# Optimization experiments

Hardware: AMD Instinct MI355X
Metric: run time of the kernel (lower is better)

The kernel has to match this reference:

```python
import jax, jax.numpy as jnp
import numpy as np
import math

V, S, D, C, L = 32000, 1024, 768, 6, 4
B = 32
PAD = 0
EPS = 1e-5


def _ln(x, w, b):
    m = jnp.mean(x, axis=-1, keepdims=True)
    v = jnp.var(x, axis=-1, keepdims=True)
    return (x - m) * jax.lax.rsqrt(v + EPS) * w + b


def setup_inputs() -> dict:
    key = jax.random.key(0)
    ks = jax.random.split(key, 20)
    s = 0.02
    emb = jax.random.normal(ks[0], (V, D), jnp.float32) * s
    emb = emb.at[PAD].set(0.0)  # padding_idx row zeroed
    pos_emb = jax.random.normal(ks[1], (S, D), jnp.float32) * s
    tokens = jax.random.randint(ks[2], (B, S), 0, V)
    d = dict(
        tokens=tokens,
        emb=emb,
        pos_emb=pos_emb,
        ln1_w=jnp.ones((L, D)), ln1_b=jnp.zeros((L, D)),
        ln2_w=jnp.ones((L, D)), ln2_b=jnp.zeros((L, D)),
        wq=jax.random.normal(ks[3], (L, D, D)) * s, bq=jnp.zeros((L, D)),
        wk=jax.random.normal(ks[4], (L, D, D)) * s, bk=jnp.zeros((L, D)),
        wv=jax.random.normal(ks[5], (L, D, D)) * s, bv=jnp.zeros((L, D)),
        w1=jax.random.normal(ks[6], (L, D, 2 * D)) * s, b1=jnp.zeros((L, 2 * D)),
        w2=jax.random.normal(ks[7], (L, 2 * D, D)) * s, b2=jnp.zeros((L, D)),
        lnf_w=jnp.ones((D,)), lnf_b=jnp.zeros((D,)),
        wc=jax.random.normal(ks[8], (D, C)) * s, bc=jnp.zeros((C,)),
    )
    return d


def reference(tokens, emb, pos_emb, ln1_w, ln1_b, ln2_w, ln2_b,
              wq, bq, wk, bk, wv, bv, w1, b1, w2, b2,
              lnf_w, lnf_b, wc, bc):
    # dropout in eval mode -> identity
    seq = tokens.shape[1]
    x = emb[tokens] + pos_emb[jnp.arange(seq)][None]  # [B,S,D]
    pad = (tokens == PAD)[:, None, :]  # [B,1,S] mask over key positions
    scale = math.sqrt(D)
    for l in range(L):
        n = _ln(x, ln1_w[l], ln1_b[l])
        q = n @ wq[l] + bq[l]
        k = n @ wk[l] + bk[l]
        v = n @ wv[l] + bv[l]
        scores = jnp.einsum('bqd,bkd->bqk', q, k) / scale
        scores = jnp.where(pad, -jnp.inf, scores)
        attn = jax.nn.softmax(scores, axis=-1)
        x = x + jnp.einsum('bqk,bkd->bqd', attn, v)
        h = jax.nn.relu(_ln(x, ln2_w[l], ln2_b[l]) @ w1[l] + b1[l])
        x = x + h @ w2[l] + b2[l]
    x = _ln(x, lnf_w, lnf_b)
    tok_mask = (tokens != PAD)[..., None].astype(x.dtype)  # [B,S,1]
    pooled = (x * tok_mask).sum(axis=1) / jnp.clip(tok_mask.sum(axis=1), 1.0, None)
    return pooled @ wc + bc
```

## Files before the change

### kernel.cpp

```cpp
#include <hip/hip_runtime.h>
#include <hip/hip_bf16.h>


typedef float f32x4 __attribute__((ext_vector_type(4)));
typedef unsigned short u16x4 __attribute__((ext_vector_type(4)));
typedef unsigned short u16x8 __attribute__((ext_vector_type(8)));
typedef int   i32x4 __attribute__((ext_vector_type(4)));
typedef __bf16 bf16x8 __attribute__((ext_vector_type(8)));

#define NB  32
#define NS  1024
#define ND  768
#define NH  1536
#define NL  4
#define NM  (NB * NS)

__device__ __forceinline__ unsigned short f2bf(float f) {
    unsigned u = __builtin_bit_cast(unsigned, f);
    unsigned r = (u + 0x7FFFu + ((u >> 16) & 1u)) >> 16;
    return (unsigned short)r;
}
__device__ __forceinline__ float bf2f(unsigned short h) {
    return __builtin_bit_cast(float, (unsigned)h << 16);
}
__device__ __forceinline__ unsigned short f2h(float f) {
    _Float16 h = (_Float16)f;
    return __builtin_bit_cast(unsigned short, h);
}
__device__ __forceinline__ float h2f(unsigned short u) {
    _Float16 h = __builtin_bit_cast(_Float16, u);
    return (float)h;
}

__device__ __forceinline__ void gl_lds16(const void* g, void* l) {
    __builtin_amdgcn_global_load_lds(
        (const __attribute__((address_space(1))) unsigned int*)g,
        (__attribute__((address_space(3))) unsigned int*)l, 16, 0, 0);
}

__global__ void embed_kernel(const int* __restrict__ tok,
                             const float* __restrict__ emb,
                             const float* __restrict__ pos,
                             unsigned short* __restrict__ x) {
    const int row = blockIdx.x;
    const int c = threadIdx.x;
    const int tk = tok[row];
    const int s = row & (NS - 1);
    f32x4 e = *(const f32x4*)(emb + (size_t)tk * ND + c * 4);
    f32x4 p = *(const f32x4*)(pos + (size_t)s * ND + c * 4);
    u16x4 o;
    #pragma unroll
    for (int i = 0; i < 4; i++) o[i] = f2h(e[i] + p[i]);
    *(u16x4*)(x + (size_t)row * ND + c * 4) = o;
}

__global__ __launch_bounds__(256)
void wt_kernel(const float* __restrict__ in, unsigned short* __restrict__ out,
               int R, int Cc, size_t ozs) {
    __shared__ float ls[64][65];
    const int t = threadIdx.x;
    const size_t zi = (size_t)blockIdx.z * R * Cc;
    const size_t zo = (size_t)blockIdx.z * ozs;
    const int r0 = blockIdx.y * 64, c0 = blockIdx.x * 64;
    #pragma unroll
    for (int i = 0; i < 4; i++) {
        const int r = i * 16 + (t >> 4);
        const int c = (t & 15) * 4;
        f32x4 v = *(const f32x4*)(in + zi + (size_t)(r0 + r) * Cc + c0 + c);
        ls[r][c] = v[0]; ls[r][c + 1] = v[1]; ls[r][c + 2] = v[2]; ls[r][c + 3] = v[3];
    }
    __syncthreads();
    #pragma unroll
    for (int i = 0; i < 2; i++) {
        const int c = i * 32 + (t >> 3);
        const int r = (t & 7) * 8;
        u16x8 o;
        #pragma unroll
        for (int j = 0; j < 8; j++) o[j] = f2bf(ls[r + j][c]);
        *(u16x8*)(out + zo + (size_t)(c0 + c) * R + r0 + r) = o;
    }
}

__global__ void bcat_kernel(const float* __restrict__ bq, const float* __restrict__ bk,
                            float* __restrict__ bqk) {
    const int i = blockIdx.x * 256 + threadIdx.x;
    const int l = i / NH, j = i % NH;
    bqk[i] = (j < ND) ? bq[l * ND + j] : bk[l * ND + j - ND];
}

__global__ __launch_bounds__(256)
void ln_kernel(const unsigned short* __restrict__ x, const float* __restrict__ g,
               const float* __restrict__ bta, unsigned short* __restrict__ out) {
    const int row = blockIdx.x * 4 + (threadIdx.x >> 6);
    const int l = threadIdx.x & 63;
    const unsigned short* xr = x + (size_t)row * ND;
    f32x4 vv[3];
    float s = 0.f, ss = 0.f;
    #pragma unroll
    for (int j = 0; j < 3; j++) {
        u16x4 hv = *(const u16x4*)(xr + (j * 64 + l) * 4);
        #pragma unroll
        for (int i = 0; i < 4; i++) {
            vv[j][i] = h2f(hv[i]);
            s += vv[j][i]; ss += vv[j][i] * vv[j][i];
        }
    }
    #pragma unroll
    for (int off = 32; off >= 1; off >>= 1) {
        s += __shfl_xor(s, off); ss += __shfl_xor(ss, off);
    }
    const float mean = s * (1.0f / ND);
    const float var = ss * (1.0f / ND) - mean * mean;
    const float rstd = rsqrtf(var + 1e-5f);
    #pragma unroll
    for (int j = 0; j < 3; j++) {
        const int c = (j * 64 + l) * 4;
        f32x4 gv = *(const f32x4*)(g + c);
        f32x4 bv = *(const f32x4*)(bta + c);
        u16x4 o;
        #pragma unroll
        for (int i = 0; i < 4; i++) o[i] = f2bf((vv[j][i] - mean) * rstd * gv[i] + bv[i]);
        *(u16x4*)(out + (size_t)row * ND + c) = o;
    }
}

template<int EPI, int BROW>
__global__ __launch_bounds__(512, 2)
void gemm256_kernel(const unsigned short* __restrict__ A,
                    const unsigned short* __restrict__ Bt,
                    const float* __restrict__ bias,
                    void* __restrict__ Cv,
                    int N, int K, int lda, int ldb,
                    long sA, long sB, long sC, float scale, int doswz) {
    __shared__ unsigned short lds[65536];
    const int tid = threadIdx.x;
    const int wid = tid >> 6, l = tid & 63;
    const int wr = wid >> 2, wc = wid & 3;
    const int fr = l & 15, fq = l >> 4;

    int bn = blockIdx.x, bm = blockIdx.y, bz = blockIdx.z;
    if (doswz) {
        const int gx = gridDim.x, gy = gridDim.y;
        const int nwg = gx * gy * gridDim.z;
        const int flat = (bz * gy + bm) * gx + bn;
        int s = (flat & 7) * (nwg >> 3) + (flat >> 3);
        bn = s % gx; s /= gx; bm = s % gy; bz = s / gy;
    }

    const unsigned short* Ab = A + (size_t)bz * sA + (size_t)(bm * 256) * lda;
    const unsigned short* Bb = Bt + (size_t)bz * sB + (size_t)(bn * 256) * ldb;

    const int srow = tid >> 3;
    const int scol = ((tid & 7) ^ (srow & 7)) * 8;
    const unsigned ldst = (unsigned)wid * 1024u;

    auto stageA = [&](int kt, int h) {
        const unsigned base = (unsigned)(kt & 1) * 65536u + (unsigned)h * 16384u;
        #pragma unroll
        for (int li = 0; li < 2; li++)
            gl_lds16(Ab + (size_t)(h * 128 + li * 64 + srow) * lda + (kt * 64 + scol),
                     (char*)lds + base + (unsigned)li * 8192u + ldst);
    };
    auto stageB = [&](int kt, int h) {
        const unsigned base = (unsigned)(kt & 1) * 65536u + 32768u + (unsigned)h * 16384u;
        #pragma unroll
        for (int li = 0; li < 2; li++)
            gl_lds16(Bb + (size_t)(h * 128 + li * 64 + srow) * ldb + (kt * 64 + scol),
                     (char*)lds + base + (unsigned)li * 8192u + ldst);
    };
    auto ldaf = [&](int buf, int mi, int kk) -> bf16x8 {
        const unsigned r = (unsigned)(mi * 16 + fr);
        unsigned byt = r * 128u + (unsigned)kk * 64u + (unsigned)fq * 16u;
        byt ^= (r & 7u) << 4;
        return *(const bf16x8*)((const char*)lds +
            (unsigned)buf * 65536u + (unsigned)wr * 16384u + byt);
    };
    auto ldbf = [&](int buf, int ni, int kk) -> bf16x8 {
        const unsigned r = (unsigned)((wc & 1) * 64 + ni * 16 + fr);
        unsigned byt = r * 128u + (unsigned)kk * 64u + (unsigned)fq * 16u;
        byt ^= (r & 7u) << 4;
        return *(const bf16x8*)((const char*)lds +
            (unsigned)buf * 65536u + 32768u + (unsigned)(wc >> 1) * 16384u + byt);
    };

    const int NT = K >> 6;
    f32x4 acc[8][4] = {};

    stageB(0, 0); stageB(0, 1); stageA(0, 0); stageA(0, 1);
    if (NT > 1) {
        stageB(1, 0); stageB(1, 1);
        asm volatile("s_waitcnt vmcnt(4)" ::: "memory");
    } else {
        asm volatile("s_waitcnt vmcnt(0)" ::: "memory");
    }
    __builtin_amdgcn_s_barrier();
    __builtin_amdgcn_sched_barrier(0);

    for (int t = 0; t < NT; ++t) {
        const int cur = t & 1;
        bf16x8 bfr[8];
        #pragma unroll
        for (int ni = 0; ni < 4; ni++) {
            bfr[ni * 2 + 0] = ldbf(cur, ni, 0);
            bfr[ni * 2 + 1] = ldbf(cur, ni, 1);
        }
        #pragma unroll
        for (int p = 0; p < 4; p++) {
            bf16x8 a0 = ldaf(cur, 2 * p,     0);
            bf16x8 a1 = ldaf(cur, 2 * p,     1);
            bf16x8 a2 = ldaf(cur, 2 * p + 1, 0);
            bf16x8 a3 = ldaf(cur, 2 * p + 1, 1);
            if (p < 2) { if (t + 1 < NT) stageA(t + 1, p); }
            else       { if (t + 2 < NT) stageB(t + 2, p - 2); }
            if (p == 3) {
                if (t + 2 < NT) asm volatile("s_waitcnt vmcnt(4)" ::: "memory");
                else            asm volatile("s_waitcnt vmcnt(0)" ::: "memory");
            }
            __builtin_amdgcn_s_barrier();
            asm volatile("s_waitcnt lgkmcnt(0)" ::: "memory");
            __builtin_amdgcn_sched_barrier(0);
            __builtin_amdgcn_s_setprio(1);
            #pragma unroll
            for (int ni = 0; ni < 4; ni++) {
                acc[2 * p][ni] = __builtin_amdgcn_mfma_f32_16x16x32_bf16(
                    a0, bfr[ni * 2 + 0], acc[2 * p][ni], 0, 0, 0);
                acc[2 * p][ni] = __builtin_amdgcn_mfma_f32_16x16x32_bf16(
                    a1, bfr[ni * 2 + 1], acc[2 * p][ni], 0, 0, 0);
                acc[2 * p + 1][ni] = __builtin_amdgcn_mfma_f32_16x16x32_bf16(
                    a2, bfr[ni * 2 + 0], acc[2 * p + 1][ni], 0, 0, 0);
                acc[2 * p + 1][ni] = __builtin_amdgcn_mfma_f32_16x16x32_bf16(
                    a3, bfr[ni * 2 + 1], acc[2 * p + 1][ni], 0, 0, 0);
            }
            __builtin_amdgcn_s_setprio(0);
            __builtin_amdgcn_sched_barrier(0);
            __builtin_amdgcn_s_barrier();
            __builtin_amdgcn_sched_barrier(0);
        }
    }

    const int erow = tid >> 4;
    const int echk = tid & 15;
    #pragma unroll
    for (int h2 = 0; h2 < 2; ++h2) {
        __builtin_amdgcn_s_barrier();
        if (wr == h2) {
            #pragma unroll
            for (int mi = 0; mi < 8; mi++) {
                #pragma unroll
                for (int ni = 0; ni < 4; ni++) {
                    const int nl = wc * 64 + ni * 16 + fr;
                    const float bcol = (!BROW && bias) ? bias[bn * 256 + nl] : 0.0f;
                    f32x4 brow = {0, 0, 0, 0};
                    if (BROW) brow = *(const f32x4*)(bias + bm * 256 + h2 * 128 + mi * 16 + fq * 4);
                    #pragma unroll
                    for (int r = 0; r < 4; r++) {
                        const int lm = mi * 16 + fq * 4 + r;
                        float v = acc[mi][ni][r] * scale + (BROW ? brow[r] : bcol);
                        if (EPI == 1) v = fmaxf(v, 0.0f);
                        const unsigned byt = ((unsigned)lm * 1024u + (unsigned)nl * 4u)
                                             ^ ((unsigned)(lm & 7) << 4);
                        *(float*)((char*)lds + byt) = v;
                    }
                }
            }
        }
        __builtin_amdgcn_s_barrier();
        #pragma unroll
        for (int j = 0; j < 16; j++) {
            const int row = erow + 32 * (j >> 2);
            const int c   = echk + 16 * (j & 3);
            const unsigned byt = ((unsigned)row * 1024u + (unsigned)c * 16u)
                                 ^ ((unsigned)(row & 7) << 4);
            f32x4 v = *(const f32x4*)((const char*)lds + byt);
            const int m = bm * 256 + h2 * 128 + row;
            const int ncol = bn * 256 + c * 4;
            const size_t offc = (size_t)bz * sC + (size_t)m * N + ncol;
            if (EPI == 2) {
                unsigned short* cp = (unsigned short*)Cv + offc;
                u16x4 hv = *(const u16x4*)cp;
                u16x4 o;
                #pragma unroll
                for (int r = 0; r < 4; r++) o[r] = f2h(h2f(hv[r]) + v[r]);
                *(u16x4*)cp = o;
            } else {
                u16x4 o;
                o[0] = f2bf(v[0]); o[1] = f2bf(v[1]); o[2] = f2bf(v[2]); o[3] = f2bf(v[3]);
                *(u16x4*)((unsigned short*)Cv + offc) = o;
            }
        }
    }
}

__global__ __launch_bounds__(256)
void softmax_kernel(unsigned short* __restrict__ sc, const int* __restrict__ tokg) {
    const int row = blockIdx.x * 4 + (threadIdx.x >> 6);
    const int l = threadIdx.x & 63;
    const int b = row >> 10;
    unsigned short* rp = sc + (size_t)row * NS;
    const int* trow = tokg + (size_t)b * NS;
    float v[16];
    float mx = -3.4e38f;
    #pragma unroll
    for (int j = 0; j < 2; j++) {
        u16x8 u = *(const u16x8*)(rp + j * 512 + l * 8);
        i32x4 t0 = *(const i32x4*)(trow + j * 512 + l * 8);
        i32x4 t1 = *(const i32x4*)(trow + j * 512 + l * 8 + 4);
        #pragma unroll
        for (int i = 0; i < 8; i++) {
            const int tk = (i < 4) ? t0[i] : t1[i - 4];
            const float s = (tk == 0) ? -__builtin_inff() : bf2f(u[i]);
            v[j * 8 + i] = s;
            mx = fmaxf(mx, s);
        }
    }
    #pragma unroll
    for (int off = 32; off >= 1; off >>= 1) mx = fmaxf(mx, __shfl_xor(mx, off));
    float sum = 0.f;
    #pragma unroll
    for (int i = 0; i < 16; i++) { v[i] = __expf(v[i] - mx); sum += v[i]; }
    #pragma unroll
    for (int off = 32; off >= 1; off >>= 1) sum += __shfl_xor(sum, off);
    const float inv = 1.0f / sum;
    #pragma unroll
    for (int j = 0; j < 2; j++) {
        u16x8 o;
        #pragma unroll
        for (int i = 0; i < 8; i++) o[i] = f2bf(v[j * 8 + i] * inv);
        *(u16x8*)(rp + j * 512 + l * 8) = o;
    }
}

__global__ __launch_bounds__(256)
void pool1_kernel(const unsigned short* __restrict__ ln,
                  const int* __restrict__ tokg,
                  float* __restrict__ part, float* __restrict__ cnts,
                  int gbase) {
    const int d = blockIdx.x * 256 + threadIdx.x;
    const int b = blockIdx.y;
    const int z = blockIdx.z;
    float s = 0.f, cnt = 0.f;
    const int i0 = z * 128;
    for (int i = i0; i < i0 + 128; i++) {
        const int tk = tokg[b * NS + i];
        if (tk != 0) { s += bf2f(ln[((size_t)b * NS + i) * ND + d]); cnt += 1.0f; }
    }
    part[((size_t)z * NB + (gbase + b)) * ND + d] = s;
    if (d == 0) cnts[z * NB + (gbase + b)] = cnt;
}

__global__ __launch_bounds__(256)
void pool2_kernel(const float* __restrict__ part, const float* __restrict__ cnts,
                  float* __restrict__ pooled) {
    const int d = blockIdx.x * 256 + threadIdx.x;
    const int b = blockIdx.y;
    float s = 0.f, cnt = 0.f;
    #pragma unroll
    for (int z = 0; z < 8; z++) {
        s += part[((size_t)z * NB + b) * ND + d];
        cnt += cnts[z * NB + b];
    }
    pooled[(size_t)b * ND + d] = s / fmaxf(cnt, 1.0f);
}

__global__ void cls_kernel(const float* __restrict__ pooled, const float* __restrict__ wc,
                           const float* __restrict__ bc, float* __restrict__ out) {
    const int b = blockIdx.x;
    const int l = threadIdx.x;
    float a[6] = {0, 0, 0, 0, 0, 0};
    for (int d = l; d < ND; d += 64) {
        const float p = pooled[b * ND + d];
        #pragma unroll
        for (int c = 0; c < 6; c++) a[c] += p * wc[d * 6 + c];
    }
    #pragma unroll
    for (int c = 0; c < 6; c++) {
        #pragma unroll
        for (int off = 32; off >= 1; off >>= 1) a[c] += __shfl_xor(a[c], off);
    }
    if (l == 0) {
        #pragma unroll
        for (int c = 0; c < 6; c++) out[b * 6 + c] = a[c] + bc[c];
    }
}

__global__ void zero_out_kernel(float* out, int nel) {
    const int i = blockIdx.x * 256 + threadIdx.x;
    if (i < nel) out[i] = 0.0f;
}

extern "C" void kernel_launch(void* const* d_in, const int* in_sizes, int n_in,
                              void* d_out, int out_size, void* d_ws, size_t ws_size,
                              hipStream_t stream) {
    const int*   tok  = (const int*)d_in[0];
    const float* emb  = (const float*)d_in[1];
    const float* pos  = (const float*)d_in[2];
    const float* ln1w = (const float*)d_in[3];
    const float* ln1b = (const float*)d_in[4];
    const float* ln2w = (const float*)d_in[5];
    const float* ln2b = (const float*)d_in[6];
    const float* wq   = (const float*)d_in[7];
    const float* bq   = (const float*)d_in[8];
    const float* wk   = (const float*)d_in[9];
    const float* bk   = (const float*)d_in[10];
    const float* wv   = (const float*)d_in[11];
    const float* bv   = (const float*)d_in[12];
    const float* w1   = (const float*)d_in[13];
    const float* b1   = (const float*)d_in[14];
    const float* w2   = (const float*)d_in[15];
    const float* b2   = (const float*)d_in[16];
    const float* lnfw = (const float*)d_in[17];
    const float* lnfb = (const float*)d_in[18];
    const float* wcw  = (const float*)d_in[19];
    const float* bcb  = (const float*)d_in[20];
    float* out = (float*)d_out;

    size_t off = 0;
    auto carve = [&](size_t bytes) -> char* {
        char* p = (char*)d_ws + off;
        off += (bytes + 255) & ~(size_t)255;
        return p;
    };
    unsigned short* x = (unsigned short*)carve((size_t)NM * ND * 2);
    unsigned short* wqkT = (unsigned short*)carve((size_t)NL * NH * ND * 2);
    unsigned short* wvT  = (unsigned short*)carve((size_t)NL * ND * ND * 2);
    unsigned short* w1T  = (unsigned short*)carve((size_t)NL * ND * NH * 2);
    unsigned short* w2T  = (unsigned short*)carve((size_t)NL * NH * ND * 2);
    float* bqk    = (float*)carve((size_t)NL * NH * 4);
    float* part   = (float*)carve((size_t)8 * NB * ND * 4);
    float* cnts   = (float*)carve((size_t)8 * NB * 4);
    float* pooled = (float*)carve((size_t)NB * ND * 4);

    int G = 32;
    while (G >= 1) {
        const size_t pool = (size_t)G *
            ((size_t)NS * ND * 2
           + (size_t)NS * NH * 2
           + (size_t)NS * ND * 2
           + (size_t)NS * NS * 2);
        if (off + pool <= ws_size) break;
        G >>= 1;
    }
    if (G < 1) {
        zero_out_kernel<<<(out_size + 255) / 256, 256, 0, stream>>>(out, out_size);
        return;
    }
    const int MG = G * NS;
    unsigned short* n  = (unsigned short*)carve((size_t)MG * ND * 2);
    unsigned short* qk = (unsigned short*)carve((size_t)MG * NH * 2);
    unsigned short* vt = (unsigned short*)carve((size_t)MG * ND * 2);
    unsigned short* sc = (unsigned short*)carve((size_t)G * NS * NS * 2);
    unsigned short* h  = qk;

    embed_kernel<<<NM, 192, 0, stream>>>(tok, emb, pos, x);
    wt_kernel<<<dim3(12, 12, NL), 256, 0, stream>>>(wq, wqkT,            ND, ND, (size_t)NH * ND);
    wt_kernel<<<dim3(12, 12, NL), 256, 0, stream>>>(wk, wqkT + ND * ND,  ND, ND, (size_t)NH * ND);
    wt_kernel<<<dim3(12, 12, NL), 256, 0, stream>>>(wv, wvT,             ND, ND, (size_t)ND * ND);
    wt_kernel<<<dim3(24, 12, NL), 256, 0, stream>>>(w1, w1T,             ND, NH, (size_t)ND * NH);
    wt_kernel<<<dim3(12, 24, NL), 256, 0, stream>>>(w2, w2T,             NH, ND, (size_t)NH * ND);
    bcat_kernel<<<NL * NH / 256, 256, 0, stream>>>(bq, bk, bqk);

    const float iscale = 1.0f / sqrtf((float)ND);
    const int NGroups = NB / G;
    const int MT = MG / 256;
    for (int l = 0; l < NL; l++) {
        for (int g = 0; g < NGroups; g++) {
            const size_t rowoff = (size_t)g * MG;
            unsigned short* xg = x + rowoff * ND;
            ln_kernel<<<MG / 4, 256, 0, stream>>>(xg, ln1w + l * ND, ln1b + l * ND, n);
            gemm256_kernel<0, 0><<<dim3(6, MT, 1), 512, 0, stream>>>(
                n, wqkT + (size_t)l * NH * ND, bqk + l * NH, qk,
                NH, ND, ND, ND, 0, 0, 0, 1.0f, ((6 * MT) % 8 == 0) ? 1 : 0);
            gemm256_kernel<0, 1><<<dim3(4, 3, G), 512, 0, stream>>>(
                wvT + (size_t)l * ND * ND, n, bv + l * ND, vt,
                NS, ND, ND, ND, 0, (long)NS * ND, (long)ND * NS, 1.0f,
                ((12 * G) % 8 == 0) ? 1 : 0);
            gemm256_kernel<0, 0><<<dim3(4, 4, G), 512, 0, stream>>>(
                qk, qk + ND, nullptr, sc,
                NS, ND, NH, NH, (long)NS * NH, (long)NS * NH, (long)NS * NS, iscale,
                ((16 * G) % 8 == 0) ? 1 : 0);
            softmax_kernel<<<MG / 4, 256, 0, stream>>>(sc, tok + rowoff);
            gemm256_kernel<2, 0><<<dim3(3, 4, G), 512, 0, stream>>>(
                sc, vt, nullptr, xg,
                ND, NS, NS, NS, (long)NS * NS, (long)ND * NS, (long)NS * ND, 1.0f,
                ((12 * G) % 8 == 0) ? 1 : 0);
            ln_kernel<<<MG / 4, 256, 0, stream>>>(xg, ln2w + l * ND, ln2b + l * ND, n);
            gemm256_kernel<1, 0><<<dim3(6, MT, 1), 512, 0, stream>>>(
                n, w1T + (size_t)l * ND * NH, b1 + l * NH, h,
                NH, ND, ND, ND, 0, 0, 0, 1.0f, ((6 * MT) % 8 == 0) ? 1 : 0);
            gemm256_kernel<2, 0><<<dim3(3, MT, 1), 512, 0, stream>>>(
                h, w2T + (size_t)l * ND * NH, b2 + l * ND, xg,
                ND, NH, NH, NH, 0, 0, 0, 1.0f, ((3 * MT) % 8 == 0) ? 1 : 0);
        }
    }
    for (int g = 0; g < NGroups; g++) {
        const size_t rowoff = (size_t)g * MG;
        ln_kernel<<<MG / 4, 256, 0, stream>>>(x + rowoff * ND, lnfw, lnfb, n);
        pool1_kernel<<<dim3(3, G, 8), 256, 0, stream>>>(n, tok + rowoff, part, cnts, g * G);
    }
    pool2_kernel<<<dim3(3, NB), 256, 0, stream>>>(part, cnts, pooled);
    cls_kernel<<<NB, 64, 0, stream>>>(pooled, wcw, bcb, out);
}
```

Measured before the change: 2.563 ms.

## Triple-buffer A tiles in LDS and prefetch A two k-steps ahead

The GEMM's A operand moves from double to triple buffering in LDS, so A tiles are now prefetched two k-iterations ahead like B, with rotating read and write slots. LDS grows to 160KB, and the waitcnt thresholds are raised so more global-to-LDS loads can be in flight. The goal is to hide more global memory latency behind the MFMA work. In exchange, the prologue always stages two tiles, which assumes K is at least 128, and the larger LDS footprint rules out running two blocks per CU.

```diff
diff --git a/kernel.cpp b/kernel.cpp
--- a/kernel.cpp
+++ b/kernel.cpp
@@ -132,7 +132,7 @@
                     void* __restrict__ Cv,
                     int N, int K, int lda, int ldb,
                     long sA, long sB, long sC, float scale, int doswz) {
-    __shared__ unsigned short lds[65536];
+    __shared__ __align__(16) unsigned char lds[163840];
     const int tid = threadIdx.x;
     const int wid = tid >> 6, l = tid & 63;
     const int wr = wid >> 2, wc = wid & 3;
@@ -154,66 +154,65 @@
     const int scol = ((tid & 7) ^ (srow & 7)) * 8;
     const unsigned ldst = (unsigned)wid * 1024u;
 
-    auto stageA = [&](int kt, int h) {
-        const unsigned base = (unsigned)(kt & 1) * 65536u + (unsigned)h * 16384u;
+    auto stageA = [&](unsigned bbase, int kt, int h) {
         #pragma unroll
         for (int li = 0; li < 2; li++)
             gl_lds16(Ab + (size_t)(h * 128 + li * 64 + srow) * lda + (kt * 64 + scol),
-                     (char*)lds + base + (unsigned)li * 8192u + ldst);
+                     lds + bbase + (unsigned)h * 16384u + (unsigned)li * 8192u + ldst);
     };
-    auto stageB = [&](int kt, int h) {
-        const unsigned base = (unsigned)(kt & 1) * 65536u + 32768u + (unsigned)h * 16384u;
+    auto stageB = [&](unsigned bbase, int kt, int h) {
         #pragma unroll
         for (int li = 0; li < 2; li++)
             gl_lds16(Bb + (size_t)(h * 128 + li * 64 + srow) * ldb + (kt * 64 + scol),
-                     (char*)lds + base + (unsigned)li * 8192u + ldst);
+                     lds + bbase + (unsigned)h * 16384u + (unsigned)li * 8192u + ldst);
     };
-    auto ldaf = [&](int buf, int mi, int kk) -> bf16x8 {
+    auto ldaf = [&](unsigned bbase, int mi, int kk) -> bf16x8 {
         const unsigned r = (unsigned)(mi * 16 + fr);
         unsigned byt = r * 128u + (unsigned)kk * 64u + (unsigned)fq * 16u;
         byt ^= (r & 7u) << 4;
-        return *(const bf16x8*)((const char*)lds +
-            (unsigned)buf * 65536u + (unsigned)wr * 16384u + byt);
+        return *(const bf16x8*)(lds + bbase + (unsigned)wr * 16384u + byt);
     };
-    auto ldbf = [&](int buf, int ni, int kk) -> bf16x8 {
+    auto ldbf = [&](unsigned bbase, int ni, int kk) -> bf16x8 {
         const unsigned r = (unsigned)((wc & 1) * 64 + ni * 16 + fr);
         unsigned byt = r * 128u + (unsigned)kk * 64u + (unsigned)fq * 16u;
         byt ^= (r & 7u) << 4;
-        return *(const bf16x8*)((const char*)lds +
-            (unsigned)buf * 65536u + 32768u + (unsigned)(wc >> 1) * 16384u + byt);
+        return *(const bf16x8*)(lds + bbase + (unsigned)(wc >> 1) * 16384u + byt);
     };
 
     const int NT = K >> 6;
     f32x4 acc[8][4] = {};
 
-    stageB(0, 0); stageB(0, 1); stageA(0, 0); stageA(0, 1);
-    if (NT > 1) {
-        stageB(1, 0); stageB(1, 1);
-        asm volatile("s_waitcnt vmcnt(4)" ::: "memory");
-    } else {
-        asm volatile("s_waitcnt vmcnt(0)" ::: "memory");
-    }
+    stageB(98304u, 0, 0);          stageB(98304u, 0, 1);
+    stageA(0u, 0, 0);              stageA(0u, 0, 1);
+    stageB(98304u + 32768u, 1, 0); stageB(98304u + 32768u, 1, 1);
+    stageA(32768u, 1, 0);          stageA(32768u, 1, 1);
+    asm volatile("s_waitcnt vmcnt(8)" ::: "memory");
     __builtin_amdgcn_s_barrier();
     __builtin_amdgcn_sched_barrier(0);
 
+    int aRd = 0, aWr = 2;
     for (int t = 0; t < NT; ++t) {
-        const int cur = t & 1;
+        const unsigned baseA = (unsigned)aRd * 32768u;
+        const unsigned baseB = 98304u + (unsigned)(t & 1) * 32768u;
+        const unsigned stgA  = (unsigned)aWr * 32768u;
+        const unsigned stgB  = baseB;
+
         bf16x8 bfr[8];
         #pragma unroll
         for (int ni = 0; ni < 4; ni++) {
-            bfr[ni * 2 + 0] = ldbf(cur, ni, 0);
-            bfr[ni * 2 + 1] = ldbf(cur, ni, 1);
+            bfr[ni * 2 + 0] = ldbf(baseB, ni, 0);
+            bfr[ni * 2 + 1] = ldbf(baseB, ni, 1);
         }
         #pragma unroll
         for (int p = 0; p < 4; p++) {
-            bf16x8 a0 = ldaf(cur, 2 * p,     0);
-            bf16x8 a1 = ldaf(cur, 2 * p,     1);
-            bf16x8 a2 = ldaf(cur, 2 * p + 1, 0);
-            bf16x8 a3 = ldaf(cur, 2 * p + 1, 1);
-            if (p < 2) { if (t + 1 < NT) stageA(t + 1, p); }
-            else       { if (t + 2 < NT) stageB(t + 2, p - 2); }
+            bf16x8 a0 = ldaf(baseA, 2 * p,     0);
+            bf16x8 a1 = ldaf(baseA, 2 * p,     1);
+            bf16x8 a2 = ldaf(baseA, 2 * p + 1, 0);
+            bf16x8 a3 = ldaf(baseA, 2 * p + 1, 1);
+            if (p < 2) { if (t + 2 < NT) stageA(stgA, t + 2, p); }
+            else       { if (t + 2 < NT) stageB(stgB, t + 2, p - 2); }
             if (p == 3) {
-                if (t + 2 < NT) asm volatile("s_waitcnt vmcnt(4)" ::: "memory");
+                if (t + 2 < NT) asm volatile("s_waitcnt vmcnt(8)" ::: "memory");
                 else            asm volatile("s_waitcnt vmcnt(0)" ::: "memory");
             }
             __builtin_amdgcn_s_barrier();
@@ -236,6 +235,8 @@
             __builtin_amdgcn_s_barrier();
             __builtin_amdgcn_sched_barrier(0);
         }
+        aRd = (aRd == 2) ? 0 : aRd + 1;
+        aWr = (aWr == 2) ? 0 : aWr + 1;
     }
 
     const int erow = tid >> 4;
@@ -259,7 +260,7 @@
                         if (EPI == 1) v = fmaxf(v, 0.0f);
                         const unsigned byt = ((unsigned)lm * 1024u + (unsigned)nl * 4u)
                                              ^ ((unsigned)(lm & 7) << 4);
-                        *(float*)((char*)lds + byt) = v;
+                        *(float*)(lds + byt) = v;
                     }
                 }
             }
@@ -271,7 +272,7 @@
             const int c   = echk + 16 * (j & 3);
             const unsigned byt = ((unsigned)row * 1024u + (unsigned)c * 16u)
                                  ^ ((unsigned)(row & 7) << 4);
-            f32x4 v = *(const f32x4*)((const char*)lds + byt);
+            f32x4 v = *(const f32x4*)(lds + byt);
             const int m = bm * 256 + h2 * 128 + row;
             const int ncol = bn * 256 + c * 4;
             const size_t offc = (size_t)bz * sC + (size_t)m * N + ncol;
```

New measurement: 2.646 ms. +3.3%, slower.
